# Performance work log

Hardware: AMD Instinct MI355X
Metric: run time of the kernel (lower is better)

Reference implementation:

```python
import jax, jax.numpy as jnp
import numpy as np

BITS = 4
GROUP = 128
IN = 4096
OUT = 14336
B = 64
PACK = 32 // BITS          # 8 values per int32
MAXQ = (1 << BITS) - 1     # 15


def setup_inputs() -> dict:
    key = jax.random.key(0)
    k = jax.random.split(key, 5)
    x = jax.random.normal(k[0], (B, IN), dtype=jnp.float32)
    # non-negative int32 so arithmetic right-shift behaves like logical shift
    qweight = jax.random.randint(k[1], (IN // PACK, OUT), 0, 2**31 - 1, dtype=jnp.int32)
    qzeros = jax.random.randint(k[2], (IN // GROUP, OUT // PACK), 0, 2**31 - 1, dtype=jnp.int32)
    scales = jax.random.uniform(k[3], (IN // GROUP, OUT), dtype=jnp.float32,
                                minval=1e-3, maxval=1e-2)
    bias = jax.random.normal(k[4], (OUT,), dtype=jnp.float32) * 0.01
    g_idx = (jnp.arange(IN) // GROUP).astype(jnp.int32)
    return dict(x=x, qweight=qweight, qzeros=qzeros, scales=scales, bias=bias, g_idx=g_idx)


def _dequant(qweight, qzeros, scales, g_idx):
    shifts = jnp.arange(PACK, dtype=jnp.int32) * BITS  # [PACK]
    # unpack weights: [IN//PACK, PACK, OUT] -> [IN, OUT]
    w = (qweight[:, None, :] >> shifts[None, :, None]) & MAXQ
    w = w.reshape(IN, OUT)
    # unpack zeros: [G, OUT//PACK, PACK] -> [G, OUT]; pack() stored (zeros-1), so add 1 back
    z = (qzeros[:, :, None] >> shifts[None, None, :]) & MAXQ
    z = z.reshape(-1, OUT) + 1
    # per-group dequant with arbitrary g_idx (act-order support)
    return scales[g_idx] * (w - z[g_idx]).astype(scales.dtype)


def reference(x, qweight, qzeros, scales, bias, g_idx):
    W = _dequant(qweight, qzeros, scales, g_idx)  # [IN, OUT]
    return x @ W + bias
```

## Files before the change

### kernel.cpp

```cpp
#include <hip/hip_runtime.h>
#include <hip/hip_bf16.h>

using u32 = unsigned int;
using u16 = unsigned short;

typedef __attribute__((ext_vector_type(8))) _Float16 half8;
typedef __attribute__((ext_vector_type(2))) _Float16 half2v;
typedef __attribute__((ext_vector_type(16))) float f32x16;
typedef __attribute__((ext_vector_type(4))) u32 u32x4;

#define IN_K   4096
#define OUT_N  14336
#define SPLITK 4
#define NSTAGE 8
#define OUT_ELEMS (64 * OUT_N)

__global__ __launch_bounds__(256) void prep_kernel(const float* __restrict__ x,
                                                   u16* __restrict__ xs) {
  const int t = blockIdx.x * 256 + threadIdx.x;
  const int c = t >> 6;
  const int r = t & 63;
  const float* px = x + r * IN_K + c * 8;
  const float4 a = *(const float4*)px;
  const float4 b = *(const float4*)(px + 4);
  const float af[4] = {a.x, a.y, a.z, a.w};
  const float bf[4] = {b.x, b.y, b.z, b.w};
  union { u32x4 v; u32 u[4]; } o;
#pragma unroll
  for (int i = 0; i < 4; ++i) {
    const _Float16 hl = (_Float16)af[i];
    const _Float16 hh = (_Float16)bf[i];
    u16 lo, hi;
    __builtin_memcpy(&lo, &hl, 2);
    __builtin_memcpy(&hi, &hh, 2);
    o.u[i] = (u32)lo | ((u32)hi << 16);
  }
  *(u32x4*)(xs + (size_t)t * 8) = o.v;
}

__global__ __launch_bounds__(256) void bias_init_kernel(const float* __restrict__ bias,
                                                        float* __restrict__ out) {
  const int i = (blockIdx.x * 256 + threadIdx.x) * 4;
  const int col = i % OUT_N;
  *(float4*)(out + i) = *(const float4*)(bias + col);
}

__global__ __launch_bounds__(256) void reduce_kernel(const float* __restrict__ part,
                                                     const float* __restrict__ bias,
                                                     float* __restrict__ out) {
  const int i = (blockIdx.x * 256 + threadIdx.x) * 4;
  const int col = i % OUT_N;
  const float4 a0 = *(const float4*)(part + i);
  const float4 a1 = *(const float4*)(part + (size_t)OUT_ELEMS + i);
  const float4 a2 = *(const float4*)(part + 2 * (size_t)OUT_ELEMS + i);
  const float4 a3 = *(const float4*)(part + 3 * (size_t)OUT_ELEMS + i);
  const float4 bv = *(const float4*)(bias + col);
  float4 r;
  r.x = a0.x + a1.x + a2.x + a3.x + bv.x;
  r.y = a0.y + a1.y + a2.y + a3.y + bv.y;
  r.z = a0.z + a1.z + a2.z + a3.z + bv.z;
  r.w = a0.w + a1.w + a2.w + a3.w + bv.w;
  *(float4*)(out + i) = r;
}

template <bool ATOMIC>
__global__ __launch_bounds__(256, 2) void qgemm_kernel(
    const u32* __restrict__ qw, const u32* __restrict__ qz,
    const float* __restrict__ scal, const u16* __restrict__ xs,
    float* __restrict__ dst) {
  __shared__ u16 lds[2][8192];
  const int tid = threadIdx.x;
  const int lane = tid & 63;
  const int wv = tid >> 6;
  const int g = lane >> 5;
  const int nn = lane & 31;
  const int colabs = blockIdx.x * 128 + wv * 32 + nn;
  const int by = blockIdx.y;
  const int chunk0 = by * 128;

  f32x16 acc0, acc1;
#pragma unroll
  for (int i = 0; i < 16; ++i) { acc0[i] = 0.f; acc1[i] = 0.f; }

  auto issue = [&](int st) {
    const u16* src = xs + (size_t)(chunk0 + st * 16) * 512;
    u16* dstl = &lds[st & 1][0];
#pragma unroll
    for (int r = 0; r < 4; ++r) {
      const int p = r * 256 + tid;
      __builtin_amdgcn_global_load_lds(
          (const __attribute__((address_space(1))) void*)(src + p * 8),
          (__attribute__((address_space(3))) void*)(dstl + p * 8), 16, 0, 0);
    }
  };

  issue(0);
  u32 qn[8];
#pragma unroll
  for (int s = 0; s < 8; ++s)
    qn[s] = qw[(size_t)(chunk0 + 2 * s + g) * OUT_N + colabs];
  float sn = scal[(size_t)(by * 8) * OUT_N + colabs];
  u32 zn = qz[(size_t)(by * 8) * (OUT_N / 8) + (colabs >> 3)];

#pragma unroll
  for (int st = 0; st < NSTAGE; ++st) {
    u32 qc[8];
#pragma unroll
    for (int s = 0; s < 8; ++s) qc[s] = qn[s];
    const float scur = sn;
    const u32 zcur = zn;

    if (st < NSTAGE - 1) {
      __builtin_amdgcn_s_barrier();
      asm volatile("" ::: "memory");
      issue(st + 1);
      asm volatile("s_waitcnt vmcnt(4)" ::: "memory");
    } else {
      asm volatile("s_waitcnt vmcnt(0)" ::: "memory");
    }
    __builtin_amdgcn_s_barrier();
    asm volatile("" ::: "memory");

    if (st < NSTAGE - 1) {
      const int c1 = chunk0 + (st + 1) * 16;
#pragma unroll
      for (int s = 0; s < 8; ++s)
        qn[s] = qw[(size_t)(c1 + 2 * s + g) * OUT_N + colabs];
      sn = scal[(size_t)(by * 8 + st + 1) * OUT_N + colabs];
      zn = qz[(size_t)(by * 8 + st + 1) * (OUT_N / 8) + (colabs >> 3)];
    }

    const u32 zq = (zcur >> ((colabs & 7) * 4)) & 0xFu;
    const u32 hzu = 0x64016401u + zq * 0x00010001u;
    half2v hz; __builtin_memcpy(&hz, &hzu, 4);
    const _Float16 hs = (_Float16)scur;
    const half2v s2 = {hs, hs};

    const u16* buf = &lds[st & 1][0];
#pragma unroll
    for (int s = 0; s < 8; ++s) {
      const int cl = s * 2 + g;
      const half8 a0 = *(const half8*)(buf + (cl * 64 + nn) * 8);
      const half8 a1 = *(const half8*)(buf + (cl * 64 + nn + 32) * 8);
      const u32 q = qc[s];
      const u32 p0 = (q & 0x000F000Fu) | 0x64006400u;
      const u32 p1 = ((q >> 4) & 0x000F000Fu) | 0x64006400u;
      const u32 p2 = ((q >> 8) & 0x000F000Fu) | 0x64006400u;
      const u32 p3 = ((q >> 12) & 0x000F000Fu) | 0x64006400u;
      half2v t0, t1, t2, t3;
      __builtin_memcpy(&t0, &p0, 4);
      __builtin_memcpy(&t1, &p1, 4);
      __builtin_memcpy(&t2, &p2, 4);
      __builtin_memcpy(&t3, &p3, 4);
      union { half8 v; half2v h[4]; } bb;
      bb.h[0] = (t0 - hz) * s2;
      bb.h[1] = (t1 - hz) * s2;
      bb.h[2] = (t2 - hz) * s2;
      bb.h[3] = (t3 - hz) * s2;
      acc0 = __builtin_amdgcn_mfma_f32_32x32x16_f16(a0, bb.v, acc0, 0, 0, 0);
      acc1 = __builtin_amdgcn_mfma_f32_32x32x16_f16(a1, bb.v, acc1, 0, 0, 0);
    }
  }

#pragma unroll
  for (int r = 0; r < 16; ++r) {
    const int row = (r & 3) + 8 * (r >> 2) + 4 * g;
    if (ATOMIC) {
      unsafeAtomicAdd(&dst[(size_t)row * OUT_N + colabs], acc0[r]);
      unsafeAtomicAdd(&dst[(size_t)(row + 32) * OUT_N + colabs], acc1[r]);
    } else {
      float* p = dst + (size_t)by * OUT_ELEMS;
      p[(size_t)row * OUT_N + colabs] = acc0[r];
      p[(size_t)(row + 32) * OUT_N + colabs] = acc1[r];
    }
  }
}

extern "C" void kernel_launch(void* const* d_in, const int* in_sizes, int n_in,
                              void* d_out, int out_size, void* d_ws, size_t ws_size,
                              hipStream_t stream) {
  (void)in_sizes; (void)n_in; (void)out_size;
  const float* x    = (const float*)d_in[0];
  const u32*   qw   = (const u32*)d_in[1];
  const u32*   qz   = (const u32*)d_in[2];
  const float* sc   = (const float*)d_in[3];
  const float* bias = (const float*)d_in[4];
  float* out = (float*)d_out;

  const size_t XS_BYTES   = (size_t)64 * IN_K * 2;
  const size_t PART_BYTES = (size_t)SPLITK * OUT_ELEMS * 4;
  u16* xs = (u16*)d_ws;

  prep_kernel<<<128, 256, 0, stream>>>(x, xs);

  if (ws_size >= XS_BYTES + PART_BYTES) {
    float* part = (float*)((char*)d_ws + XS_BYTES);
    qgemm_kernel<false><<<dim3(112, SPLITK), 256, 0, stream>>>(qw, qz, sc, xs, part);
    reduce_kernel<<<896, 256, 0, stream>>>(part, bias, out);
  } else {
    bias_init_kernel<<<896, 256, 0, stream>>>(bias, out);
    qgemm_kernel<true><<<dim3(112, SPLITK), 256, 0, stream>>>(qw, qz, sc, xs, out);
  }
}
```

Measured before the change: 29.68 us.

## Drop LDS staging, load activations directly from global, double split-K

```diff
diff --git a/kernel.cpp b/kernel.cpp
--- a/kernel.cpp
+++ b/kernel.cpp
@@ -11,8 +11,7 @@
 
 #define IN_K   4096
 #define OUT_N  14336
-#define SPLITK 4
-#define NSTAGE 8
+#define SPLITK 8
 #define OUT_ELEMS (64 * OUT_N)
 
 __global__ __launch_bounds__(256) void prep_kernel(const float* __restrict__ x,
@@ -50,25 +49,20 @@
                                                      float* __restrict__ out) {
   const int i = (blockIdx.x * 256 + threadIdx.x) * 4;
   const int col = i % OUT_N;
-  const float4 a0 = *(const float4*)(part + i);
-  const float4 a1 = *(const float4*)(part + (size_t)OUT_ELEMS + i);
-  const float4 a2 = *(const float4*)(part + 2 * (size_t)OUT_ELEMS + i);
-  const float4 a3 = *(const float4*)(part + 3 * (size_t)OUT_ELEMS + i);
-  const float4 bv = *(const float4*)(bias + col);
-  float4 r;
-  r.x = a0.x + a1.x + a2.x + a3.x + bv.x;
-  r.y = a0.y + a1.y + a2.y + a3.y + bv.y;
-  r.z = a0.z + a1.z + a2.z + a3.z + bv.z;
-  r.w = a0.w + a1.w + a2.w + a3.w + bv.w;
+  float4 r = *(const float4*)(bias + col);
+#pragma unroll
+  for (int p = 0; p < SPLITK; ++p) {
+    const float4 a = *(const float4*)(part + (size_t)p * OUT_ELEMS + i);
+    r.x += a.x; r.y += a.y; r.z += a.z; r.w += a.w;
+  }
   *(float4*)(out + i) = r;
 }
 
 template <bool ATOMIC>
-__global__ __launch_bounds__(256, 2) void qgemm_kernel(
+__global__ __launch_bounds__(256, 4) void qgemm_kernel(
     const u32* __restrict__ qw, const u32* __restrict__ qz,
     const float* __restrict__ scal, const u16* __restrict__ xs,
     float* __restrict__ dst) {
-  __shared__ u16 lds[2][8192];
   const int tid = threadIdx.x;
   const int lane = tid & 63;
   const int wv = tid >> 6;
@@ -76,73 +70,45 @@
   const int nn = lane & 31;
   const int colabs = blockIdx.x * 128 + wv * 32 + nn;
   const int by = blockIdx.y;
-  const int chunk0 = by * 128;
+  const int r0 = by * 64 + g;
+  const int grp0 = by * 4;
+  const int zsh = (colabs & 7) * 4;
+
+  const u16* pa = xs + ((size_t)r0 * 64 + nn) * 8;
+  const u32* pq = qw + (size_t)r0 * OUT_N + colabs;
 
   f32x16 acc0, acc1;
 #pragma unroll
   for (int i = 0; i < 16; ++i) { acc0[i] = 0.f; acc1[i] = 0.f; }
 
-  auto issue = [&](int st) {
-    const u16* src = xs + (size_t)(chunk0 + st * 16) * 512;
-    u16* dstl = &lds[st & 1][0];
-#pragma unroll
-    for (int r = 0; r < 4; ++r) {
-      const int p = r * 256 + tid;
-      __builtin_amdgcn_global_load_lds(
-          (const __attribute__((address_space(1))) void*)(src + p * 8),
-          (__attribute__((address_space(3))) void*)(dstl + p * 8), 16, 0, 0);
-    }
-  };
-
-  issue(0);
-  u32 qn[8];
-#pragma unroll
-  for (int s = 0; s < 8; ++s)
-    qn[s] = qw[(size_t)(chunk0 + 2 * s + g) * OUT_N + colabs];
-  float sn = scal[(size_t)(by * 8) * OUT_N + colabs];
-  u32 zn = qz[(size_t)(by * 8) * (OUT_N / 8) + (colabs >> 3)];
+  half8 a0 = *(const half8*)pa;
+  half8 a1 = *(const half8*)(pa + 256);
+  u32 q = *pq;
+  float sc_c = scal[(size_t)grp0 * OUT_N + colabs];
+  u32 zw_c = qz[(size_t)grp0 * (OUT_N / 8) + (colabs >> 3)];
 
 #pragma unroll
-  for (int st = 0; st < NSTAGE; ++st) {
-    u32 qc[8];
-#pragma unroll
-    for (int s = 0; s < 8; ++s) qc[s] = qn[s];
-    const float scur = sn;
-    const u32 zcur = zn;
-
-    if (st < NSTAGE - 1) {
-      __builtin_amdgcn_s_barrier();
-      asm volatile("" ::: "memory");
-      issue(st + 1);
-      asm volatile("s_waitcnt vmcnt(4)" ::: "memory");
-    } else {
-      asm volatile("s_waitcnt vmcnt(0)" ::: "memory");
-    }
-    __builtin_amdgcn_s_barrier();
-    asm volatile("" ::: "memory");
-
-    if (st < NSTAGE - 1) {
-      const int c1 = chunk0 + (st + 1) * 16;
-#pragma unroll
-      for (int s = 0; s < 8; ++s)
-        qn[s] = qw[(size_t)(c1 + 2 * s + g) * OUT_N + colabs];
-      sn = scal[(size_t)(by * 8 + st + 1) * OUT_N + colabs];
-      zn = qz[(size_t)(by * 8 + st + 1) * (OUT_N / 8) + (colabs >> 3)];
-    }
-
-    const u32 zq = (zcur >> ((colabs & 7) * 4)) & 0xFu;
+  for (int grp = 0; grp < 4; ++grp) {
+    const u32 zq = (zw_c >> zsh) & 0xFu;
     const u32 hzu = 0x64016401u + zq * 0x00010001u;
     half2v hz; __builtin_memcpy(&hz, &hzu, 4);
-    const _Float16 hs = (_Float16)scur;
+    const _Float16 hs = (_Float16)sc_c;
     const half2v s2 = {hs, hs};
-
-    const u16* buf = &lds[st & 1][0];
+    if (grp < 3) {
+      sc_c = scal[(size_t)(grp0 + grp + 1) * OUT_N + colabs];
+      zw_c = qz[(size_t)(grp0 + grp + 1) * (OUT_N / 8) + (colabs >> 3)];
+    }
 #pragma unroll
     for (int s = 0; s < 8; ++s) {
-      const int cl = s * 2 + g;
-      const half8 a0 = *(const half8*)(buf + (cl * 64 + nn) * 8);
-      const half8 a1 = *(const half8*)(buf + (cl * 64 + nn + 32) * 8);
-      const u32 q = qc[s];
+      const int t = grp * 8 + s;
+      half8 a0n = {}, a1n = {};
+      u32 qn = 0;
+      if (t < 31) {
+        const u16* pan = pa + (size_t)(t + 1) * 1024;
+        a0n = *(const half8*)pan;
+        a1n = *(const half8*)(pan + 256);
+        qn = pq[(size_t)(t + 1) * 2 * OUT_N];
+      }
       const u32 p0 = (q & 0x000F000Fu) | 0x64006400u;
       const u32 p1 = ((q >> 4) & 0x000F000Fu) | 0x64006400u;
       const u32 p2 = ((q >> 8) & 0x000F000Fu) | 0x64006400u;
@@ -159,6 +125,7 @@
       bb.h[3] = (t3 - hz) * s2;
       acc0 = __builtin_amdgcn_mfma_f32_32x32x16_f16(a0, bb.v, acc0, 0, 0, 0);
       acc1 = __builtin_amdgcn_mfma_f32_32x32x16_f16(a1, bb.v, acc1, 0, 0, 0);
+      a0 = a0n; a1 = a1n; q = qn;
     }
   }
 
```

Result: slower. 33.46 us (+12.7%).

## Double split-K, prefetch weights two stages ahead, raise occupancy and MFMA priority

Applied to the files above, without the earlier changes.

```diff
diff --git a/kernel.cpp b/kernel.cpp
--- a/kernel.cpp
+++ b/kernel.cpp
@@ -11,8 +11,8 @@
 
 #define IN_K   4096
 #define OUT_N  14336
-#define SPLITK 4
-#define NSTAGE 8
+#define SPLITK 8
+#define NSTAGE 4
 #define OUT_ELEMS (64 * OUT_N)
 
 __global__ __launch_bounds__(256) void prep_kernel(const float* __restrict__ x,
@@ -50,21 +50,17 @@
                                                      float* __restrict__ out) {
   const int i = (blockIdx.x * 256 + threadIdx.x) * 4;
   const int col = i % OUT_N;
-  const float4 a0 = *(const float4*)(part + i);
-  const float4 a1 = *(const float4*)(part + (size_t)OUT_ELEMS + i);
-  const float4 a2 = *(const float4*)(part + 2 * (size_t)OUT_ELEMS + i);
-  const float4 a3 = *(const float4*)(part + 3 * (size_t)OUT_ELEMS + i);
-  const float4 bv = *(const float4*)(bias + col);
-  float4 r;
-  r.x = a0.x + a1.x + a2.x + a3.x + bv.x;
-  r.y = a0.y + a1.y + a2.y + a3.y + bv.y;
-  r.z = a0.z + a1.z + a2.z + a3.z + bv.z;
-  r.w = a0.w + a1.w + a2.w + a3.w + bv.w;
+  float4 r = *(const float4*)(bias + col);
+#pragma unroll
+  for (int p = 0; p < SPLITK; ++p) {
+    const float4 a = *(const float4*)(part + (size_t)p * OUT_ELEMS + i);
+    r.x += a.x; r.y += a.y; r.z += a.z; r.w += a.w;
+  }
   *(float4*)(out + i) = r;
 }
 
 template <bool ATOMIC>
-__global__ __launch_bounds__(256, 2) void qgemm_kernel(
+__global__ __launch_bounds__(256, 3) void qgemm_kernel(
     const u32* __restrict__ qw, const u32* __restrict__ qz,
     const float* __restrict__ scal, const u16* __restrict__ xs,
     float* __restrict__ dst) {
@@ -76,7 +72,9 @@
   const int nn = lane & 31;
   const int colabs = blockIdx.x * 128 + wv * 32 + nn;
   const int by = blockIdx.y;
-  const int chunk0 = by * 128;
+  const int chunk0 = by * 64;
+  const int grp0 = by * 4;
+  const int zsh = (colabs & 7) * 4;
 
   f32x16 acc0, acc1;
 #pragma unroll
@@ -93,50 +91,52 @@
           (__attribute__((address_space(3))) void*)(dstl + p * 8), 16, 0, 0);
     }
   };
-
+  auto loadQ = [&](int st, u32* qr, float& sr, u32& zr) {
+    const int c = chunk0 + st * 16;
+#pragma unroll
+    for (int s = 0; s < 8; ++s)
+      qr[s] = qw[(size_t)(c + 2 * s + g) * OUT_N + colabs];
+    sr = scal[(size_t)(grp0 + st) * OUT_N + colabs];
+    zr = qz[(size_t)(grp0 + st) * (OUT_N / 8) + (colabs >> 3)];
+  };
+
+  u32 qbuf[2][8]; float sbuf[2]; u32 zbuf[2];
   issue(0);
-  u32 qn[8];
-#pragma unroll
-  for (int s = 0; s < 8; ++s)
-    qn[s] = qw[(size_t)(chunk0 + 2 * s + g) * OUT_N + colabs];
-  float sn = scal[(size_t)(by * 8) * OUT_N + colabs];
-  u32 zn = qz[(size_t)(by * 8) * (OUT_N / 8) + (colabs >> 3)];
+  loadQ(0, qbuf[0], sbuf[0], zbuf[0]);
+  loadQ(1, qbuf[1], sbuf[1], zbuf[1]);
 
 #pragma unroll
   for (int st = 0; st < NSTAGE; ++st) {
-    u32 qc[8];
-#pragma unroll
-    for (int s = 0; s < 8; ++s) qc[s] = qn[s];
-    const float scur = sn;
-    const u32 zcur = zn;
-
     if (st < NSTAGE - 1) {
       __builtin_amdgcn_s_barrier();
       asm volatile("" ::: "memory");
       issue(st + 1);
-      asm volatile("s_waitcnt vmcnt(4)" ::: "memory");
+      if (st < NSTAGE - 2)
+        asm volatile("s_waitcnt vmcnt(14)" ::: "memory");
+      else
+        asm volatile("s_waitcnt vmcnt(4)" ::: "memory");
     } else {
       asm volatile("s_waitcnt vmcnt(0)" ::: "memory");
     }
     __builtin_amdgcn_s_barrier();
     asm volatile("" ::: "memory");
 
-    if (st < NSTAGE - 1) {
-      const int c1 = chunk0 + (st + 1) * 16;
-#pragma unroll
-      for (int s = 0; s < 8; ++s)
-        qn[s] = qw[(size_t)(c1 + 2 * s + g) * OUT_N + colabs];
-      sn = scal[(size_t)(by * 8 + st + 1) * OUT_N + colabs];
-      zn = qz[(size_t)(by * 8 + st + 1) * (OUT_N / 8) + (colabs >> 3)];
-    }
-
-    const u32 zq = (zcur >> ((colabs & 7) * 4)) & 0xFu;
+    u32 qc[8];
+#pragma unroll
+    for (int s = 0; s < 8; ++s) qc[s] = qbuf[st & 1][s];
+    const float scur = sbuf[st & 1];
+    const u32 zcur = zbuf[st & 1];
+    if (st < NSTAGE - 2)
+      loadQ(st + 2, qbuf[st & 1], sbuf[st & 1], zbuf[st & 1]);
+
+    const u32 zq = (zcur >> zsh) & 0xFu;
     const u32 hzu = 0x64016401u + zq * 0x00010001u;
     half2v hz; __builtin_memcpy(&hz, &hzu, 4);
     const _Float16 hs = (_Float16)scur;
     const half2v s2 = {hs, hs};
 
     const u16* buf = &lds[st & 1][0];
+    __builtin_amdgcn_s_setprio(1);
 #pragma unroll
     for (int s = 0; s < 8; ++s) {
       const int cl = s * 2 + g;
@@ -160,6 +160,7 @@
       acc0 = __builtin_amdgcn_mfma_f32_32x32x16_f16(a0, bb.v, acc0, 0, 0, 0);
       acc1 = __builtin_amdgcn_mfma_f32_32x32x16_f16(a1, bb.v, acc1, 0, 0, 0);
     }
+    __builtin_amdgcn_s_setprio(0);
   }
 
 #pragma unroll
```

New measurement: 32.62 us. 1.1x slower.
